# Kernel tuning notes

Measured on AMD Instinct MI355X. Metric: run time of the kernel, lower is better.

The kernel has to match this reference:

```python
import jax, jax.numpy as jnp
import numpy as np

TEMPERATURE = 0.5
EPS = 1e-8  # F.cosine_similarity eps


def _neg_mask_indices(B):
    # mask: ones, zero diagonal, zero the two positive off-diagonals
    N = 2 * B
    mask = np.ones((N, N), dtype=bool)
    np.fill_diagonal(mask, False)
    idx = np.arange(B)
    mask[idx, idx + B] = False
    mask[idx + B, idx] = False
    rows, cols = np.nonzero(mask)  # static, computed at trace time
    return rows, cols


def setup_inputs() -> dict:
    key = jax.random.key(0)
    k1, k2 = jax.random.split(key)
    B, D = 4096, 128
    z_i = jax.random.normal(k1, (B, D), dtype=jnp.float32)
    z_j = jax.random.normal(k2, (B, D), dtype=jnp.float32)
    return {"z_i": z_i, "z_j": z_j}


def reference(z_i, z_j):
    B = z_i.shape[0]
    N = 2 * B
    z = jnp.concatenate([z_i, z_j], axis=0)  # [N, D]
    norm = jnp.maximum(jnp.linalg.norm(z, axis=1, keepdims=True), EPS)
    zn = z / norm
    sim = (zn @ zn.T) / TEMPERATURE  # [N, N] cosine similarity / temp

    # positives: the i <-> i+B pairs
    sim_i_j = jnp.diagonal(sim, offset=B)
    sim_j_i = jnp.diagonal(sim, offset=-B)
    positives = jnp.concatenate([sim_i_j, sim_j_i], axis=0)[:, None]  # [N, 1]

    rows, cols = _neg_mask_indices(B)
    negatives = sim[rows, cols].reshape(N, N - 2)  # [N, N-2]

    logits = jnp.concatenate([positives, negatives], axis=1)  # [N, N-1]
    # cross-entropy with labels == 0 (positive is column 0)
    loss = jnp.mean(jax.nn.logsumexp(logits, axis=1) - logits[:, 0])
    return loss
```

## Files before the change

kernel.cpp:

```cpp
#include <hip/hip_runtime.h>
#include <hip/hip_bf16.h>
#include <math.h>


typedef __attribute__((ext_vector_type(8))) short bf16x8;
typedef __attribute__((ext_vector_type(4))) float f32x4;

#define NROWS 8192
#define DDIM  128
#define BHALF 4096
#define CHUNK 32
#define COLS_PER_STRIP 512
#define EXP2SCALE 2.8853900817779268f

static __device__ __forceinline__ unsigned short f2bf(float f) {
  unsigned int u = __float_as_uint(f);
  unsigned int r = (u + 0x7fffu + ((u >> 16) & 1u)) >> 16;
  return (unsigned short)r;
}

static __device__ __forceinline__ void glds16(const unsigned short* g, unsigned short* l) {
  __builtin_amdgcn_global_load_lds((const __attribute__((address_space(1))) unsigned int*)g,
                                   (__attribute__((address_space(3))) unsigned int*)l,
                                   16, 0, 0);
}

__global__ void norm_zero_kernel(const float* __restrict__ zi, const float* __restrict__ zj,
                                 unsigned short* __restrict__ zn,
                                 float* __restrict__ row_sums, float* __restrict__ out) {
  int wave = threadIdx.x >> 6;
  int lane = threadIdx.x & 63;
  int row  = blockIdx.x * 4 + wave;
  const float* src = (row < BHALF) ? (zi + (size_t)row * DDIM)
                                   : (zj + (size_t)(row - BHALF) * DDIM);
  float2 v = *(const float2*)(src + 2 * lane);
  float ss = v.x * v.x + v.y * v.y;
  #pragma unroll
  for (int off = 1; off < 64; off <<= 1) ss += __shfl_xor(ss, off);
  float scale = 1.0f / fmaxf(sqrtf(ss), 1e-8f);
  unsigned int lo = f2bf(v.x * scale);
  unsigned int hi = f2bf(v.y * scale);
  ((unsigned int*)(zn + (size_t)row * DDIM))[lane] = lo | (hi << 16);

  if (threadIdx.x < 4) row_sums[blockIdx.x * 4 + threadIdx.x] = 0.0f;
  if (blockIdx.x == 0 && threadIdx.x == 0) out[0] = 0.0f;
}

__global__ __launch_bounds__(256, 2)
void sim_kernel(const unsigned short* __restrict__ zn, float* __restrict__ row_sums) {
  __shared__ unsigned short lds[2 * CHUNK * DDIM];

  const int wave = threadIdx.x >> 6;
  const int lane = threadIdx.x & 63;
  const int l15  = lane & 15;
  const int quad = lane >> 4;

  const int row_base  = blockIdx.x * 256 + wave * 64;
  const int col_strip = blockIdx.y * COLS_PER_STRIP;

  bf16x8 a[4][4];
  const unsigned short* abase = zn + (size_t)(row_base + l15) * DDIM + quad * 8;
  #pragma unroll
  for (int mi = 0; mi < 4; ++mi)
    #pragma unroll
    for (int kf = 0; kf < 4; ++kf)
      a[mi][kf] = *(const bf16x8*)(abase + mi * 16 * DDIM + kf * 32);

  float rs[4][4];
  #pragma unroll
  for (int mi = 0; mi < 4; ++mi)
    #pragma unroll
    for (int r = 0; r < 4; ++r) rs[mi][r] = 0.0f;

  const int t0 = wave * 64 + lane;
  const int r0 = t0 >> 4, c0 = (t0 & 15) ^ (r0 & 15);
  const int r1 = (t0 + 256) >> 4, c1 = (t0 & 15) ^ (r1 & 15);
  const unsigned short* gst0 = zn + (size_t)(col_strip + r0) * DDIM + c0 * 8;
  const unsigned short* gst1 = zn + (size_t)(col_strip + r1) * DDIM + c1 * 8;
  unsigned short* lst0 = lds + wave * 512;
  unsigned short* lst1 = lds + 2048 + wave * 512;

  int rdoff[4];
  #pragma unroll
  for (int kf = 0; kf < 4; ++kf)
    rdoff[kf] = l15 * DDIM + (((quad + 4 * kf) ^ l15) << 3);

  glds16(gst0, lst0);
  glds16(gst1, lst1 - 2048 + 2048);
  __syncthreads();

  for (int ch = 0; ch < 16; ++ch) {
    const int buf = ch & 1;
    if (ch < 15) {
      const unsigned short* g0 = gst0 + (size_t)(ch + 1) * CHUNK * DDIM;
      const unsigned short* g1 = gst1 + (size_t)(ch + 1) * CHUNK * DDIM;
      unsigned short* lb = lds + ((ch + 1) & 1) * 4096;
      glds16(g0, lb + wave * 512);
      glds16(g1, lb + 2048 + wave * 512);
    }
    const unsigned short* lb = lds + buf * 4096;
    #pragma unroll
    for (int ni = 0; ni < 2; ++ni) {
      bf16x8 b[4];
      #pragma unroll
      for (int kf = 0; kf < 4; ++kf)
        b[kf] = *(const bf16x8*)(lb + ni * 16 * DDIM + rdoff[kf]);
      f32x4 acc[4];
      #pragma unroll
      for (int mi = 0; mi < 4; ++mi) {
        f32x4 z = {0.0f, 0.0f, 0.0f, 0.0f};
        acc[mi] = __builtin_amdgcn_mfma_f32_16x16x32_bf16(a[mi][0], b[0], z, 0, 0, 0);
      }
      #pragma unroll
      for (int kf = 1; kf < 4; ++kf)
        #pragma unroll
        for (int mi = 0; mi < 4; ++mi)
          acc[mi] = __builtin_amdgcn_mfma_f32_16x16x32_bf16(a[mi][kf], b[kf], acc[mi], 0, 0, 0);
      #pragma unroll
      for (int mi = 0; mi < 4; ++mi)
        #pragma unroll
        for (int r = 0; r < 4; ++r)
          rs[mi][r] += __builtin_amdgcn_exp2f(acc[mi][r] * EXP2SCALE);
    }
    __syncthreads();
  }

  #pragma unroll
  for (int mi = 0; mi < 4; ++mi)
    #pragma unroll
    for (int r = 0; r < 4; ++r) {
      float v = rs[mi][r];
      v += __shfl_xor(v, 1);
      v += __shfl_xor(v, 2);
      v += __shfl_xor(v, 4);
      v += __shfl_xor(v, 8);
      if (l15 == 0)
        atomicAdd(&row_sums[row_base + mi * 16 + quad * 4 + r], v);
    }
}

__global__ void finalize_kernel(const unsigned short* __restrict__ zn,
                                const float* __restrict__ row_sums,
                                float* __restrict__ out) {
  int wave = threadIdx.x >> 6;
  int lane = threadIdx.x & 63;
  int i = blockIdx.x * 4 + wave;
  int p = i + BHALF;
  unsigned int ua = ((const unsigned int*)(zn + (size_t)i * DDIM))[lane];
  unsigned int ub = ((const unsigned int*)(zn + (size_t)p * DDIM))[lane];
  float d = __uint_as_float(ua << 16) * __uint_as_float(ub << 16)
          + __uint_as_float(ua & 0xffff0000u) * __uint_as_float(ub & 0xffff0000u);
  #pragma unroll
  for (int off = 1; off < 64; off <<= 1) d += __shfl_xor(d, off);

  __shared__ float red[4];
  if (lane == 0) {
    const float EXPDIAG = 7.38905609893065f;
    float si = row_sums[i] - EXPDIAG;
    float sp = row_sums[p] - EXPDIAG;
    red[wave] = logf(si) + logf(sp) - 4.0f * d;
  }
  __syncthreads();
  if (threadIdx.x == 0)
    atomicAdd(out, (red[0] + red[1] + red[2] + red[3]) * (1.0f / 8192.0f));
}

extern "C" void kernel_launch(void* const* d_in, const int* in_sizes, int n_in,
                              void* d_out, int out_size, void* d_ws, size_t ws_size,
                              hipStream_t stream) {
  const float* zi = (const float*)d_in[0];
  const float* zj = (const float*)d_in[1];
  unsigned short* zn = (unsigned short*)d_ws;
  float* row_sums = (float*)((char*)d_ws + (size_t)NROWS * DDIM * 2);
  float* out = (float*)d_out;

  norm_zero_kernel<<<2048, 256, 0, stream>>>(zi, zj, zn, row_sums, out);
  sim_kernel<<<dim3(32, 16), 256, 0, stream>>>(zn, row_sums);
  finalize_kernel<<<1024, 256, 0, stream>>>(zn, row_sums, out);
}
```

Baseline: 96.03 us.

## Exploit similarity matrix symmetry: compute upper-triangle tiles and add column sums

The sim kernel now computes only the upper-triangle 256x256 tiles of the symmetric similarity matrix. Each off-diagonal tile adds its exp values both to its row sums and, through LDS column-sum atomics, to the row sums of the mirrored rows. This roughly halves the MFMA and exp work. It also folds the exp2 scale into the normalized vectors, which removes one multiply per element. The cost is extra shuffles and LDS and global atomics per chunk, plus load imbalance, because half the launched blocks exit at once.

```diff
diff --git a/kernel.cpp b/kernel.cpp
--- a/kernel.cpp
+++ b/kernel.cpp
@@ -10,8 +10,8 @@
 #define DDIM  128
 #define BHALF 4096
 #define CHUNK 32
-#define COLS_PER_STRIP 512
-#define EXP2SCALE 2.8853900817779268f
+#define SQRT_E2S 1.6986435980707531f
+#define TWO_LN2  1.3862943611198906f
 
 static __device__ __forceinline__ unsigned short f2bf(float f) {
   unsigned int u = __float_as_uint(f);
@@ -37,7 +37,7 @@
   float ss = v.x * v.x + v.y * v.y;
   #pragma unroll
   for (int off = 1; off < 64; off <<= 1) ss += __shfl_xor(ss, off);
-  float scale = 1.0f / fmaxf(sqrtf(ss), 1e-8f);
+  float scale = SQRT_E2S / fmaxf(sqrtf(ss), 1e-8f);
   unsigned int lo = f2bf(v.x * scale);
   unsigned int hi = f2bf(v.y * scale);
   ((unsigned int*)(zn + (size_t)row * DDIM))[lane] = lo | (hi << 16);
@@ -48,15 +48,21 @@
 
 __global__ __launch_bounds__(256, 2)
 void sim_kernel(const unsigned short* __restrict__ zn, float* __restrict__ row_sums) {
+  if (blockIdx.y < blockIdx.x) return;
+  const bool diag = (blockIdx.x == blockIdx.y);
+
   __shared__ unsigned short lds[2 * CHUNK * DDIM];
+  __shared__ float colsum[256];
 
   const int wave = threadIdx.x >> 6;
   const int lane = threadIdx.x & 63;
   const int l15  = lane & 15;
   const int quad = lane >> 4;
 
-  const int row_base  = blockIdx.x * 256 + wave * 64;
-  const int col_strip = blockIdx.y * COLS_PER_STRIP;
+  const int row_base = blockIdx.x * 256 + wave * 64;
+  const int col_base = blockIdx.y * 256;
+
+  colsum[threadIdx.x] = 0.0f;
 
   bf16x8 a[4][4];
   const unsigned short* abase = zn + (size_t)(row_base + l15) * DDIM + quad * 8;
@@ -73,25 +79,23 @@
     for (int r = 0; r < 4; ++r) rs[mi][r] = 0.0f;
 
   const int t0 = wave * 64 + lane;
-  const int r0 = t0 >> 4, c0 = (t0 & 15) ^ (r0 & 15);
+  const int r0 = t0 >> 4,         c0 = (t0 & 15) ^ (r0 & 15);
   const int r1 = (t0 + 256) >> 4, c1 = (t0 & 15) ^ (r1 & 15);
-  const unsigned short* gst0 = zn + (size_t)(col_strip + r0) * DDIM + c0 * 8;
-  const unsigned short* gst1 = zn + (size_t)(col_strip + r1) * DDIM + c1 * 8;
-  unsigned short* lst0 = lds + wave * 512;
-  unsigned short* lst1 = lds + 2048 + wave * 512;
+  const unsigned short* gst0 = zn + (size_t)(col_base + r0) * DDIM + c0 * 8;
+  const unsigned short* gst1 = zn + (size_t)(col_base + r1) * DDIM + c1 * 8;
 
   int rdoff[4];
   #pragma unroll
   for (int kf = 0; kf < 4; ++kf)
     rdoff[kf] = l15 * DDIM + (((quad + 4 * kf) ^ l15) << 3);
 
-  glds16(gst0, lst0);
-  glds16(gst1, lst1 - 2048 + 2048);
+  glds16(gst0, lds + wave * 512);
+  glds16(gst1, lds + 2048 + wave * 512);
   __syncthreads();
 
-  for (int ch = 0; ch < 16; ++ch) {
+  for (int ch = 0; ch < 8; ++ch) {
     const int buf = ch & 1;
-    if (ch < 15) {
+    if (ch < 7) {
       const unsigned short* g0 = gst0 + (size_t)(ch + 1) * CHUNK * DDIM;
       const unsigned short* g1 = gst1 + (size_t)(ch + 1) * CHUNK * DDIM;
       unsigned short* lb = lds + ((ch + 1) & 1) * 4096;
@@ -116,11 +120,21 @@
         #pragma unroll
         for (int mi = 0; mi < 4; ++mi)
           acc[mi] = __builtin_amdgcn_mfma_f32_16x16x32_bf16(a[mi][kf], b[kf], acc[mi], 0, 0, 0);
+      float cs = 0.0f;
       #pragma unroll
       for (int mi = 0; mi < 4; ++mi)
         #pragma unroll
-        for (int r = 0; r < 4; ++r)
-          rs[mi][r] += __builtin_amdgcn_exp2f(acc[mi][r] * EXP2SCALE);
+        for (int r = 0; r < 4; ++r) {
+          float e = __builtin_amdgcn_exp2f(acc[mi][r]);
+          rs[mi][r] += e;
+          cs += e;
+        }
+      if (!diag) {
+        cs += __shfl_xor(cs, 16);
+        cs += __shfl_xor(cs, 32);
+        if (quad == 0)
+          atomicAdd(&colsum[(ch * 2 + ni) * 16 + l15], cs);
+      }
     }
     __syncthreads();
   }
@@ -137,6 +151,8 @@
       if (l15 == 0)
         atomicAdd(&row_sums[row_base + mi * 16 + quad * 4 + r], v);
     }
+  if (!diag)
+    atomicAdd(&row_sums[col_base + threadIdx.x], colsum[threadIdx.x]);
 }
 
 __global__ void finalize_kernel(const unsigned short* __restrict__ zn,
@@ -158,7 +174,7 @@
     const float EXPDIAG = 7.38905609893065f;
     float si = row_sums[i] - EXPDIAG;
     float sp = row_sums[p] - EXPDIAG;
-    red[wave] = logf(si) + logf(sp) - 4.0f * d;
+    red[wave] = logf(si) + logf(sp) - TWO_LN2 * d;
   }
   __syncthreads();
   if (threadIdx.x == 0)
@@ -175,6 +191,6 @@
   float* out = (float*)d_out;
 
   norm_zero_kernel<<<2048, 256, 0, stream>>>(zi, zj, zn, row_sums, out);
-  sim_kernel<<<dim3(32, 16), 256, 0, stream>>>(zn, row_sums);
+  sim_kernel<<<dim3(32, 32), 256, 0, stream>>>(zn, row_sums);
   finalize_kernel<<<1024, 256, 0, stream>>>(zn, row_sums, out);
 }
```

Result: slower. 104.0 us (+8.3%).
